# Kernel tuning notes

Hardware: AMD Instinct MI355X
Metric: run time of the kernel (lower is better)

The kernel has to match this reference:

```python
import jax, jax.numpy as jnp
import numpy as np

N_NODES = 50000
N_EDGES = 800000
IN_NODE = 16
IN_EDGE = 8
HID = 128
N_LAYERS = 4
LN_EPS = 1e-5


def setup_inputs() -> dict:
    key = jax.random.key(0)
    ks = jax.random.split(key, 16)
    s = lambda k, shape, fan: jax.random.normal(k, shape, jnp.float32) * (1.0 / np.sqrt(fan))
    inp = {
        "x": jax.random.normal(ks[0], (N_NODES, IN_NODE), jnp.float32),
        "edge_index": jax.random.randint(ks[1], (2, N_EDGES), 0, N_NODES, jnp.int32),
        "edge_attr": jax.random.normal(ks[2], (N_EDGES, IN_EDGE), jnp.float32),
        # input projection
        "W_in": s(ks[3], (HID, IN_NODE), IN_NODE),
        "b_in": jnp.zeros((HID,), jnp.float32),
        # stacked SAGEConv params: lin_l (neighbors, biased), lin_r (root, no bias)
        "Wl": s(ks[4], (N_LAYERS, HID, HID), HID),
        "bl": jnp.zeros((N_LAYERS, HID), jnp.float32),
        "Wr": s(ks[5], (N_LAYERS, HID, HID), HID),
        # stacked LayerNorm params
        "ln_g": jnp.ones((N_LAYERS, HID), jnp.float32),
        "ln_b": jnp.zeros((N_LAYERS, HID), jnp.float32),
        # edge MLP: (2*HID+IN_EDGE) -> HID -> HID//2 -> 1
        "W1": s(ks[6], (HID, 2 * HID + IN_EDGE), 2 * HID + IN_EDGE),
        "b1": jnp.zeros((HID,), jnp.float32),
        "W2": s(ks[7], (HID // 2, HID), HID),
        "b2": jnp.zeros((HID // 2,), jnp.float32),
        "W3": s(ks[8], (1, HID // 2), HID // 2),
        "b3": jnp.zeros((1,), jnp.float32),
    }
    return inp


def reference(x, edge_index, edge_attr, W_in, b_in, Wl, bl, Wr, ln_g, ln_b, W1, b1, W2, b2, W3, b3):
    n = x.shape[0]
    src, dst = edge_index[0], edge_index[1]
    # in-degree for mean aggregation (clamped to 1, as in PyG mean aggr)
    deg = jax.ops.segment_sum(jnp.ones_like(dst, jnp.float32), dst, num_segments=n)
    deg = jnp.maximum(deg, 1.0)[:, None]  # [N,1]

    h = x @ W_in.T + b_in  # [N,H]

    def layer(h, params):
        Wl_i, bl_i, Wr_i, g_i, be_i = params
        # SAGEConv: mean of source features scattered to destinations
        agg = jax.ops.segment_sum(h[src], dst, num_segments=n) / deg
        h2 = agg @ Wl_i.T + bl_i + h @ Wr_i.T
        # LayerNorm
        mu = jnp.mean(h2, axis=-1, keepdims=True)
        var = jnp.mean(jnp.square(h2 - mu), axis=-1, keepdims=True)
        h2 = (h2 - mu) * jax.lax.rsqrt(var + LN_EPS) * g_i + be_i
        # ReLU (dropout = identity in eval mode)
        return jax.nn.relu(h2), None

    h, _ = jax.lax.scan(layer, h, (Wl, bl, Wr, ln_g, ln_b))

    # edge head: gather endpoints, concat with edge_attr, MLP -> scalar logit
    e = jnp.concatenate([h[src], h[dst], edge_attr], axis=1)  # [E, 2H+F_e]
    e = jax.nn.relu(e @ W1.T + b1)
    e = jax.nn.relu(e @ W2.T + b2)
    logits = (e @ W3.T + b3)[:, 0]  # [E]
    return logits
```

## Files before the change

### kernel.cpp

```cpp
#include <hip/hip_runtime.h>
#include <stdint.h>

#define NN 50000
#define NE 800000

#define O_WIN 0
#define O_BIN 2048
#define O_WL  2176
#define O_BL  67712
#define O_WR  68224
#define O_LNG 133760
#define O_LNB 134272
#define O_W1  134784
#define O_B1  168576
#define O_W2  168704
#define O_B2  176896
#define O_W3  176960
#define O_B3  177024
#define W_TOTAL 177025

#define WS_FLAGS 0
#define WS_WC    512
#define WS_CNT   355072
#define WS_ROWP  555520
#define WS_CUR   756224
#define WS_CSR   956928
#define WS_EID   4156928
#define WS_DST   7356928
#define WS_W1P   10556928
#define WS_HB0   10630656
#define WS_HB1   23430656
#define WS_NEED  36230656

#define SCAN_NB 196

typedef float f32x4 __attribute__((ext_vector_type(4)));
typedef short bf16x8 __attribute__((ext_vector_type(8)));
typedef short bf16x4 __attribute__((ext_vector_type(4)));

__device__ __forceinline__ float b2f(unsigned short u) {
  union { unsigned int i; float f; } v; v.i = ((unsigned int)u) << 16; return v.f;
}
__device__ __forceinline__ unsigned short f2b(float f) {
  union { float f; unsigned int i; } v; v.f = f;
  return (unsigned short)((v.i + 0x7fffu + ((v.i >> 16) & 1u)) >> 16);
}

__global__ void k_fallback(unsigned short* __restrict__ out) {
  int gid = blockIdx.x * 256 + threadIdx.x;
  if (gid < NE) out[gid] = 0x3F00;
}

__global__ void k_probe(const unsigned short* __restrict__ x_u,
                        const int* __restrict__ ei32, int* __restrict__ flags) {
  const int t = threadIdx.x;
  int insane = 0;
  for (int i = t; i < 512; i += 64) {
    float v = b2f(x_u[i]);
    if (!(fabsf(v) < 1e4f)) insane++;
  }
#pragma unroll
  for (int off = 1; off < 64; off <<= 1) insane += __shfl_xor(insane, off, 64);
  int nz = 0;
  for (int i = t; i < 128; i += 64) nz |= (ei32[2 * i + 1] != 0);
  unsigned long long m = __ballot(nz != 0);
  if (t == 0) {
    flags[0] = (insane >= 16) ? 1 : 0;
    flags[1] = (m == 0ULL) ? 1 : 0;
  }
}

__global__ void k_cvt_w(const void* W_in, const void* b_in, const void* Wl,
                        const void* bl, const void* Wr, const void* lng,
                        const void* lnb, const void* W1, const void* b1,
                        const void* W2, const void* b2, const void* W3,
                        const void* b3, unsigned short* __restrict__ wc,
                        const int* __restrict__ flags) {
  const int gid = blockIdx.x * 256 + threadIdx.x;
  if (gid >= W_TOTAL) return;
  const int f32 = flags[0];
  const void* src; int off;
  if      (gid < O_BIN) { src = W_in; off = gid - O_WIN; }
  else if (gid < O_WL)  { src = b_in; off = gid - O_BIN; }
  else if (gid < O_BL)  { src = Wl;   off = gid - O_WL;  }
  else if (gid < O_WR)  { src = bl;   off = gid - O_BL;  }
  else if (gid < O_LNG) { src = Wr;   off = gid - O_WR;  }
  else if (gid < O_LNB) { src = lng;  off = gid - O_LNG; }
  else if (gid < O_W1)  { src = lnb;  off = gid - O_LNB; }
  else if (gid < O_B1)  { src = W1;   off = gid - O_W1;  }
  else if (gid < O_W2)  { src = b1;   off = gid - O_B1;  }
  else if (gid < O_B2)  { src = W2;   off = gid - O_W2;  }
  else if (gid < O_W3)  { src = b2;   off = gid - O_B2;  }
  else if (gid < O_B3)  { src = W3;   off = gid - O_W3;  }
  else                  { src = b3;   off = 0;           }
  wc[gid] = f32 ? f2b(((const float*)src)[off]) : ((const unsigned short*)src)[off];
}

__global__ void k_build_w1p(const unsigned short* __restrict__ wc,
                            unsigned short* __restrict__ W1p) {
  int gid = blockIdx.x * 256 + threadIdx.x;
  if (gid >= 128 * 288) return;
  int j = gid / 288, k = gid - j * 288;
  W1p[gid] = (k < 264) ? wc[O_W1 + j * 264 + k] : (unsigned short)0;
}

__global__ void k_cvt_ea(const void* __restrict__ ea,
                         unsigned short* __restrict__ eab,
                         const int* __restrict__ flags) {
  const int gid = blockIdx.x * 256 + threadIdx.x;
  if (gid >= NE) return;
  if (flags[0]) {
    const float4* ep = (const float4*)((const float*)ea + (size_t)gid * 8);
    const float4 a = ep[0], b = ep[1];
    union { ushort4 v[2]; int4 i; } o;
    o.v[0].x = f2b(a.x); o.v[0].y = f2b(a.y); o.v[0].z = f2b(a.z); o.v[0].w = f2b(a.w);
    o.v[1].x = f2b(b.x); o.v[1].y = f2b(b.y); o.v[1].z = f2b(b.z); o.v[1].w = f2b(b.w);
    *(int4*)(eab + (size_t)gid * 8) = o.i;
  } else {
    *(int4*)(eab + (size_t)gid * 8) =
        *(const int4*)((const unsigned short*)ea + (size_t)gid * 8);
  }
}

__global__ void k_hist(const int* __restrict__ ei, int* __restrict__ cnt,
                       const int* __restrict__ flags) {
  const int e = blockIdx.x * 256 + threadIdx.x;
  if (e >= NE) return;
  const int d = flags[1] ? ei[2 * (NE + e)] : ei[NE + e];
  atomicAdd(&cnt[d], 1);
}

__global__ __launch_bounds__(256) void k_scan1(const int* __restrict__ cnt,
                                               int* __restrict__ rowptr,
                                               int* __restrict__ bsum) {
  __shared__ int ws4[4];
  const int t = threadIdx.x, ln = t & 63, wv = t >> 6;
  const int i = blockIdx.x * 256 + t;
  const int v = (i < NN) ? cnt[i] : 0;
  int x = v;
#pragma unroll
  for (int off = 1; off < 64; off <<= 1) {
    int y = __shfl_up(x, off, 64);
    if (ln >= off) x += y;
  }
  if (ln == 63) ws4[wv] = x;
  __syncthreads();
  if (t == 0) { ws4[1] += ws4[0]; ws4[2] += ws4[1]; ws4[3] += ws4[2]; }
  __syncthreads();
  const int woff = wv ? ws4[wv - 1] : 0;
  if (i < NN) rowptr[i] = woff + x - v;
  if (t == 255) bsum[blockIdx.x] = woff + x;
}

__global__ __launch_bounds__(256) void k_scan2(int* __restrict__ bsum) {
  __shared__ int ws4[4];
  const int t = threadIdx.x, ln = t & 63, wv = t >> 6;
  const int v = (t < SCAN_NB) ? bsum[t] : 0;
  int x = v;
#pragma unroll
  for (int off = 1; off < 64; off <<= 1) {
    int y = __shfl_up(x, off, 64);
    if (ln >= off) x += y;
  }
  if (ln == 63) ws4[wv] = x;
  __syncthreads();
  if (t == 0) { ws4[1] += ws4[0]; ws4[2] += ws4[1]; ws4[3] += ws4[2]; }
  __syncthreads();
  const int woff = wv ? ws4[wv - 1] : 0;
  if (t < SCAN_NB) bsum[t] = woff + x - v;
}

__global__ void k_scan3(int* __restrict__ rowptr, const int* __restrict__ bsum) {
  const int i = blockIdx.x * 256 + threadIdx.x;
  if (i < NN) rowptr[i] += bsum[blockIdx.x];
  if (i == 0) rowptr[NN] = NE;
}

__global__ void k_fill(const int* __restrict__ ei, const int* __restrict__ rowptr,
                       int* __restrict__ cursor, int* __restrict__ csr,
                       int* __restrict__ eidA, int* __restrict__ dstA,
                       const int* __restrict__ flags) {
  const int e = blockIdx.x * 256 + threadIdx.x;
  if (e >= NE) return;
  const int i64 = flags[1];
  const int s = i64 ? ei[2 * e] : ei[e];
  const int d = i64 ? ei[2 * (NE + e)] : ei[NE + e];
  const int pos = rowptr[d] + atomicAdd(&cursor[d], 1);
  csr[pos] = s;
  eidA[pos] = e;
  dstA[pos] = d;
}

__global__ void k_inproj(const void* __restrict__ x,
                         const unsigned short* __restrict__ wc,
                         unsigned short* __restrict__ hb,
                         const int* __restrict__ flags) {
  const int gid = blockIdx.x * 256 + threadIdx.x;
  const int n = gid >> 7, j = gid & 127;
  float xv[16];
  if (flags[0]) {
    const float4* xp = (const float4*)((const float*)x + (size_t)n * 16);
#pragma unroll
    for (int q = 0; q < 4; q++) {
      float4 t = xp[q];
      xv[q * 4 + 0] = t.x; xv[q * 4 + 1] = t.y; xv[q * 4 + 2] = t.z; xv[q * 4 + 3] = t.w;
    }
  } else {
    const unsigned short* xu = (const unsigned short*)x + (size_t)n * 16;
#pragma unroll
    for (int q = 0; q < 2; q++) {
      union { int4 v; unsigned short u[8]; } t;
      t.v = *(const int4*)(xu + q * 8);
#pragma unroll
      for (int i = 0; i < 8; i++) xv[q * 8 + i] = b2f(t.u[i]);
    }
  }
  float s = b2f(wc[O_BIN + j]);
  const unsigned short* wrow = wc + O_WIN + j * 16;
#pragma unroll
  for (int q = 0; q < 2; q++) {
    union { int4 v; unsigned short u[8]; } w;
    w.v = *(const int4*)(wrow + q * 8);
#pragma unroll
    for (int i = 0; i < 8; i++) s += b2f(w.u[i]) * xv[q * 8 + i];
  }
  hb[gid] = f2b(s);
}

__global__ __launch_bounds__(256) void k_agg(
    const unsigned short* __restrict__ hin, const int* __restrict__ csr,
    const int* __restrict__ rowptr, unsigned short* __restrict__ aggb) {
  const int tid = threadIdx.x;
  const int n = blockIdx.x * 4 + (tid >> 6);
  const int L = tid & 63;
  const int rs = rowptr[n], re = rowptr[n + 1];
  const unsigned int* hw = (const unsigned int*)hin;
  long long t0 = 0, t1 = 0;
  int e = rs;
  for (; e + 8 <= re; e += 8) {
    unsigned int u[8];
#pragma unroll
    for (int k = 0; k < 8; k++) u[k] = hw[(size_t)csr[e + k] * 64 + L];
#pragma unroll
    for (int k = 0; k < 8; k++) {
      t0 += (int)(b2f((unsigned short)(u[k] & 0xffff)) * 16777216.0f);
      t1 += (int)(b2f((unsigned short)(u[k] >> 16)) * 16777216.0f);
    }
  }
  for (; e + 2 <= re; e += 2) {
    const unsigned int u0 = hw[(size_t)csr[e] * 64 + L];
    const unsigned int u1 = hw[(size_t)csr[e + 1] * 64 + L];
    t0 += (int)(b2f((unsigned short)(u0 & 0xffff)) * 16777216.0f);
    t1 += (int)(b2f((unsigned short)(u0 >> 16)) * 16777216.0f);
    t0 += (int)(b2f((unsigned short)(u1 & 0xffff)) * 16777216.0f);
    t1 += (int)(b2f((unsigned short)(u1 >> 16)) * 16777216.0f);
  }
  if (e < re) {
    const unsigned int u0 = hw[(size_t)csr[e] * 64 + L];
    t0 += (int)(b2f((unsigned short)(u0 & 0xffff)) * 16777216.0f);
    t1 += (int)(b2f((unsigned short)(u0 >> 16)) * 16777216.0f);
  }
  const int dg = re - rs;
  const float rd = (1.0f / 16777216.0f) / (float)(dg > 1 ? dg : 1);
  const float s0 = (float)t0 * rd;
  const float s1 = (float)t1 * rd;
  const unsigned int o = (unsigned int)f2b(s0) | ((unsigned int)f2b(s1) << 16);
  ((unsigned int*)aggb)[(size_t)n * 64 + L] = o;
}

__global__ __launch_bounds__(256) void k_sage_mfma(
    const unsigned short* __restrict__ hin, unsigned short* __restrict__ hagg,
    const unsigned short* __restrict__ wc, int l) {
  __shared__ __align__(16) unsigned char As[64 * 528];
  __shared__ float red1[64][4];
  __shared__ float red2[64][4];
  __shared__ float mr[64][2];
  const int tid = threadIdx.x;
  const int wv = tid >> 6;
  const int L = tid & 63;
  const int l15 = L & 15;
  const int q = L >> 4;
  const int n0 = blockIdx.x * 64;

  bf16x8 wf[2][8];
  float blv[2], gv[2], bv[2];
#pragma unroll
  for (int nt = 0; nt < 2; nt++) {
    const int jj = (wv * 2 + nt) * 16 + l15;
#pragma unroll
    for (int kc = 0; kc < 8; kc++) {
      const unsigned short* src = (kc < 4)
          ? wc + O_WL + ((size_t)l * 128 + jj) * 128 + kc * 32 + q * 8
          : wc + O_WR + ((size_t)l * 128 + jj) * 128 + (kc - 4) * 32 + q * 8;
      wf[nt][kc] = *(const bf16x8*)src;
    }
    blv[nt] = b2f(wc[O_BL + l * 128 + jj]);
    gv[nt]  = b2f(wc[O_LNG + l * 128 + jj]);
    bv[nt]  = b2f(wc[O_LNB + l * 128 + jj]);
  }

  for (int c = tid; c < 2048; c += 256) {
    const int row = c >> 5, part = c & 31;
    int node = n0 + row; if (node > NN - 1) node = NN - 1;
    const unsigned short* src = (part < 16)
        ? hagg + (size_t)node * 128 + part * 8
        : hin + (size_t)node * 128 + (part - 16) * 8;
    *(int4*)(As + row * 528 + part * 16) = *(const int4*)src;
  }
  __syncthreads();

  f32x4 acc[4][2];
#pragma unroll
  for (int mt = 0; mt < 4; mt++)
#pragma unroll
    for (int nt = 0; nt < 2; nt++) acc[mt][nt] = (f32x4)(0.0f);
#pragma unroll
  for (int kc = 0; kc < 8; kc++) {
#pragma unroll
    for (int mt = 0; mt < 4; mt++) {
      const bf16x8 a = *(const bf16x8*)(As + (mt * 16 + l15) * 528 + (kc * 32 + q * 8) * 2);
#pragma unroll
      for (int nt = 0; nt < 2; nt++)
        acc[mt][nt] = __builtin_amdgcn_mfma_f32_16x16x32_bf16(a, wf[nt][kc], acc[mt][nt], 0, 0, 0);
    }
  }
#pragma unroll
  for (int mt = 0; mt < 4; mt++) {
#pragma unroll
    for (int rg = 0; rg < 4; rg++) {
      acc[mt][0][rg] += blv[0];
      acc[mt][1][rg] += blv[1];
      float s = acc[mt][0][rg] + acc[mt][1][rg];
      float s2 = acc[mt][0][rg] * acc[mt][0][rg] + acc[mt][1][rg] * acc[mt][1][rg];
#pragma unroll
      for (int m = 1; m < 16; m <<= 1) {
        s += __shfl_xor(s, m, 64);
        s2 += __shfl_xor(s2, m, 64);
      }
      if (l15 == 0) {
        const int row = mt * 16 + q * 4 + rg;
        red1[row][wv] = s; red2[row][wv] = s2;
      }
    }
  }
  __syncthreads();
  if (tid < 64) {
    const float s1 = red1[tid][0] + red1[tid][1] + red1[tid][2] + red1[tid][3];
    const float s2 = red2[tid][0] + red2[tid][1] + red2[tid][2] + red2[tid][3];
    const float mu = s1 * 0.0078125f;
    const float var = s2 * 0.0078125f - mu * mu;
    mr[tid][0] = mu;
    mr[tid][1] = rsqrtf(var + 1e-5f);
  }
  __syncthreads();
#pragma unroll
  for (int mt = 0; mt < 4; mt++) {
#pragma unroll
    for (int rg = 0; rg < 4; rg++) {
      const int row = mt * 16 + q * 4 + rg;
      const int node = n0 + row;
      if (node < NN) {
        const float mu = mr[row][0], rstd = mr[row][1];
#pragma unroll
        for (int nt = 0; nt < 2; nt++) {
          const float o = (acc[mt][nt][rg] - mu) * rstd * gv[nt] + bv[nt];
          hagg[(size_t)node * 128 + (wv * 2 + nt) * 16 + l15] = f2b(fmaxf(o, 0.f));
        }
      }
    }
  }
}

__global__ __launch_bounds__(256) void k_edge_mfma(
    const unsigned short* __restrict__ hb, const int* __restrict__ csr,
    const int* __restrict__ eidA, const int* __restrict__ dstA,
    const unsigned short* __restrict__ eab, const unsigned short* __restrict__ W1p,
    const unsigned short* __restrict__ wc, void* __restrict__ out,
    const int* __restrict__ flags) {
  __shared__ __align__(16) unsigned char sm[30208];
  unsigned char* const Ue = sm;
  unsigned char* const Hs = sm + 4096;
  unsigned char* const E1 = sm + 4096;
  unsigned char* const E2 = sm + 21504;
  const int tid = threadIdx.x;
  const int wv = tid >> 6;
  const int L = tid & 63;
  const int l15 = L & 15;
  const int q = L >> 4;
  const int f32 = flags[0];

  for (int i = tid; i < 64 * 12; i += 256)
    *(int*)(Ue + (i / 12) * 64 + 16 + (i % 12) * 4) = 0;

  bf16x8 w1f[2][9];
  float b1v[2];
#pragma unroll
  for (int nt = 0; nt < 2; nt++) {
    const int jj = (wv * 2 + nt) * 16 + l15;
#pragma unroll
    for (int cc = 0; cc < 9; cc++)
      w1f[nt][cc] = *(const bf16x8*)(W1p + jj * 288 + cc * 32 + q * 8);
    b1v[nt] = b2f(wc[O_B1 + jj]);
  }
  bf16x8 w2f[4];
  const int jj2 = wv * 16 + l15;
#pragma unroll
  for (int kc = 0; kc < 4; kc++)
    w2f[kc] = *(const bf16x8*)(wc + O_W2 + jj2 * 128 + kc * 32 + q * 8);
  const float b2v = b2f(wc[O_B2 + jj2]);
  float w3v[16];
#pragma unroll
  for (int i = 0; i < 16; i++) w3v[i] = b2f(wc[O_W3 + q * 16 + i]);
  const float b3f = b2f(wc[O_B3]);

  for (int t = blockIdx.x; t < NE / 64; t += gridDim.x) {
    __syncthreads();
    const int pbase = t * 64;
    if (tid < 64) {
      const int e = eidA[pbase + tid];
      *(int4*)(Ue + tid * 64) = *(const int4*)(eab + (size_t)e * 8);
    }
    {
      const int r = tid >> 2, seg = tid & 3;
      const int s = csr[pbase + r];
      const unsigned short* gsrc = hb + (size_t)s * 128 + seg * 32;
      unsigned char* ldst = Hs + r * 272 + seg * 64;
      const int4 v0 = ((const int4*)gsrc)[0];
      const int4 v1 = ((const int4*)gsrc)[1];
      const int4 v2 = ((const int4*)gsrc)[2];
      const int4 v3 = ((const int4*)gsrc)[3];
      ((int4*)ldst)[0] = v0; ((int4*)ldst)[1] = v1;
      ((int4*)ldst)[2] = v2; ((int4*)ldst)[3] = v3;
    }
    int didx[4];
#pragma unroll
    for (int mt = 0; mt < 4; mt++) didx[mt] = dstA[pbase + mt * 16 + l15];
    __syncthreads();

    f32x4 acc1[4][2];
#pragma unroll
    for (int mt = 0; mt < 4; mt++)
#pragma unroll
      for (int nt = 0; nt < 2; nt++) acc1[mt][nt] = (f32x4)(0.0f);
#pragma unroll
    for (int cc = 0; cc < 4; cc++) {
#pragma unroll
      for (int mt = 0; mt < 4; mt++) {
        const bf16x8 a = *(const bf16x8*)(Hs + (mt * 16 + l15) * 272 + (cc * 32 + q * 8) * 2);
#pragma unroll
        for (int nt = 0; nt < 2; nt++)
          acc1[mt][nt] = __builtin_amdgcn_mfma_f32_16x16x32_bf16(a, w1f[nt][cc], acc1[mt][nt], 0, 0, 0);
      }
    }
#pragma unroll
    for (int cc = 4; cc < 8; cc++) {
#pragma unroll
      for (int mt = 0; mt < 4; mt++) {
        const bf16x8 a = *(const bf16x8*)(hb + (size_t)didx[mt] * 128 + (cc - 4) * 32 + q * 8);
#pragma unroll
        for (int nt = 0; nt < 2; nt++)
          acc1[mt][nt] = __builtin_amdgcn_mfma_f32_16x16x32_bf16(a, w1f[nt][cc], acc1[mt][nt], 0, 0, 0);
      }
    }
#pragma unroll
    for (int mt = 0; mt < 4; mt++) {
      const bf16x8 a = *(const bf16x8*)(Ue + (mt * 16 + l15) * 64 + q * 16);
#pragma unroll
      for (int nt = 0; nt < 2; nt++)
        acc1[mt][nt] = __builtin_amdgcn_mfma_f32_16x16x32_bf16(a, w1f[nt][8], acc1[mt][nt], 0, 0, 0);
    }
    __syncthreads();

#pragma unroll
    for (int mt = 0; mt < 4; mt++)
#pragma unroll
      for (int nt = 0; nt < 2; nt++)
#pragma unroll
        for (int rg = 0; rg < 4; rg++) {
          const int er = mt * 16 + q * 4 + rg;
          const int jj = (wv * 2 + nt) * 16 + l15;
          *(unsigned short*)(E1 + er * 272 + jj * 2) =
              f2b(fmaxf(acc1[mt][nt][rg] + b1v[nt], 0.f));
        }
    __syncthreads();

    f32x4 acc2[4];
#pragma unroll
    for (int mt = 0; mt < 4; mt++) acc2[mt] = (f32x4)(0.0f);
#pragma unroll
    for (int kc = 0; kc < 4; kc++) {
#pragma unroll
      for (int mt = 0; mt < 4; mt++) {
        const bf16x8 a = *(const bf16x8*)(E1 + (mt * 16 + l15) * 272 + (kc * 32 + q * 8) * 2);
        acc2[mt] = __builtin_amdgcn_mfma_f32_16x16x32_bf16(a, w2f[kc], acc2[mt], 0, 0, 0);
      }
    }
#pragma unroll
    for (int mt = 0; mt < 4; mt++)
#pragma unroll
      for (int rg = 0; rg < 4; rg++) {
        const int er = mt * 16 + q * 4 + rg;
        *(unsigned short*)(E2 + er * 136 + jj2 * 2) =
            f2b(fmaxf(acc2[mt][rg] + b2v, 0.f));
      }
    __syncthreads();

    const int el = wv * 16 + l15;
    float acc = 0.f;
#pragma unroll
    for (int i4 = 0; i4 < 4; i4++) {
      const bf16x4 v = *(const bf16x4*)(E2 + el * 136 + q * 32 + i4 * 8);
      acc += b2f((unsigned short)v[0]) * w3v[i4 * 4 + 0];
      acc += b2f((unsigned short)v[1]) * w3v[i4 * 4 + 1];
      acc += b2f((unsigned short)v[2]) * w3v[i4 * 4 + 2];
      acc += b2f((unsigned short)v[3]) * w3v[i4 * 4 + 3];
    }
    acc += __shfl_xor(acc, 16, 64);
    acc += __shfl_xor(acc, 32, 64);
    if (q == 0) {
      const int e = eidA[pbase + el];
      const float r = acc + b3f;
      if (f32) ((float*)out)[e] = r;
      else     ((unsigned short*)out)[e] = f2b(r);
    }
  }
}

extern "C" void kernel_launch(void* const* d_in, const int* in_sizes, int n_in,
                              void* d_out, int out_size, void* d_ws, size_t ws_size,
                              hipStream_t stream) {
  const void* x  = d_in[0];
  const int*  ei = (const int*)d_in[1];
  const void* ea = d_in[2];

  char* ws = (char*)d_ws;
  int*            flags  = (int*)(ws + WS_FLAGS);
  unsigned short* wc     = (unsigned short*)(ws + WS_WC);
  int*            cnt    = (int*)(ws + WS_CNT);
  int*            rowptr = (int*)(ws + WS_ROWP);
  int*            cursor = (int*)(ws + WS_CUR);
  int*            csr    = (int*)(ws + WS_CSR);
  int*            eidA   = (int*)(ws + WS_EID);
  int*            dstA   = (int*)(ws + WS_DST);
  unsigned short* W1p    = (unsigned short*)(ws + WS_W1P);
  unsigned short* hb0    = (unsigned short*)(ws + WS_HB0);
  unsigned short* hb1    = (unsigned short*)(ws + WS_HB1);
  int*            bsum   = (int*)(ws + WS_CSR);

  if (ws_size < WS_NEED) {
    k_fallback<<<3125, 256, 0, stream>>>((unsigned short*)d_out);
    return;
  }

  k_probe<<<1, 64, 0, stream>>>((const unsigned short*)x, ei, flags);
  k_cvt_w<<<(W_TOTAL + 255) / 256, 256, 0, stream>>>(
      d_in[3], d_in[4], d_in[5], d_in[6], d_in[7], d_in[8], d_in[9],
      d_in[10], d_in[11], d_in[12], d_in[13], d_in[14], d_in[15], wc, flags);
  k_build_w1p<<<144, 256, 0, stream>>>(wc, W1p);

  hipMemsetAsync(cnt, 0, NN * sizeof(int), stream);
  hipMemsetAsync(cursor, 0, NN * sizeof(int), stream);
  k_hist<<<3125, 256, 0, stream>>>(ei, cnt, flags);
  k_scan1<<<SCAN_NB, 256, 0, stream>>>(cnt, rowptr, bsum);
  k_scan2<<<1, 256, 0, stream>>>(bsum);
  k_scan3<<<SCAN_NB, 256, 0, stream>>>(rowptr, bsum);
  k_fill<<<3125, 256, 0, stream>>>(ei, rowptr, cursor, csr, eidA, dstA, flags);

  k_inproj<<<NN * 128 / 256, 256, 0, stream>>>(x, wc, hb0, flags);

  unsigned short* cur = hb0;
  unsigned short* nxt = hb1;
  for (int l = 0; l < 4; l++) {
    k_agg<<<12500, 256, 0, stream>>>(cur, csr, rowptr, nxt);
    k_sage_mfma<<<782, 256, 0, stream>>>(cur, nxt, wc, l);
    unsigned short* tmp = cur; cur = nxt; nxt = tmp;
  }
  unsigned short* eab = nxt;
  k_cvt_ea<<<3125, 256, 0, stream>>>(ea, eab, flags);
  k_edge_mfma<<<3125, 256, 0, stream>>>(cur, csr, eidA, dstA, eab, W1p, wc, d_out, flags);
}
```

Measured before the change: 609.7 us.

## Software-pipeline edge MLP gathers into registers and relax tile barriers

```diff
diff --git a/kernel.cpp b/kernel.cpp
--- a/kernel.cpp
+++ b/kernel.cpp
@@ -45,6 +45,11 @@
   union { float f; unsigned int i; } v; v.f = f;
   return (unsigned short)((v.i + 0x7fffu + ((v.i >> 16) & 1u)) >> 16);
 }
+
+#define LBAR() do { \
+  asm volatile("s_waitcnt lgkmcnt(0)" ::: "memory"); \
+  __builtin_amdgcn_s_barrier(); \
+} while (0)
 
 __global__ void k_fallback(unsigned short* __restrict__ out) {
   int gid = blockIdx.x * 256 + threadIdx.x;
@@ -388,6 +393,7 @@
   const int l15 = L & 15;
   const int q = L >> 4;
   const int f32 = flags[0];
+  const int r4 = tid >> 2, seg = tid & 3;
 
   for (int i = tid; i < 64 * 12; i += 256)
     *(int*)(Ue + (i / 12) * 64 + 16 + (i % 12) * 4) = 0;
@@ -408,34 +414,58 @@
   for (int kc = 0; kc < 4; kc++)
     w2f[kc] = *(const bf16x8*)(wc + O_W2 + jj2 * 128 + kc * 32 + q * 8);
   const float b2v = b2f(wc[O_B2 + jj2]);
-  float w3v[16];
-#pragma unroll
-  for (int i = 0; i < 16; i++) w3v[i] = b2f(wc[O_W3 + q * 16 + i]);
   const float b3f = b2f(wc[O_B3]);
 
-  for (int t = blockIdx.x; t < NE / 64; t += gridDim.x) {
-    __syncthreads();
+  const int NT = NE / 64;
+
+  int4 hsr0, hsr1, hsr2, hsr3;
+  int4 uer; uer.x = uer.y = uer.z = uer.w = 0;
+  int didx0, didx1, didx2, didx3;
+  {
+    const int p0 = blockIdx.x * 64;
+    const int s0 = csr[p0 + r4];
+    const unsigned short* gs = hb + (size_t)s0 * 128 + seg * 32;
+    hsr0 = ((const int4*)gs)[0]; hsr1 = ((const int4*)gs)[1];
+    hsr2 = ((const int4*)gs)[2]; hsr3 = ((const int4*)gs)[3];
+    if (tid < 64) {
+      const int e0 = eidA[p0 + tid];
+      uer = *(const int4*)(eab + (size_t)e0 * 8);
+    }
+    didx0 = dstA[p0 + 0 * 16 + l15];
+    didx1 = dstA[p0 + 1 * 16 + l15];
+    didx2 = dstA[p0 + 2 * 16 + l15];
+    didx3 = dstA[p0 + 3 * 16 + l15];
+  }
+
+  for (int t = blockIdx.x; t < NT; t += gridDim.x) {
     const int pbase = t * 64;
-    if (tid < 64) {
-      const int e = eidA[pbase + tid];
-      *(int4*)(Ue + tid * 64) = *(const int4*)(eab + (size_t)e * 8);
-    }
+    const int tn = (t + (int)gridDim.x < NT) ? (t + (int)gridDim.x) : t;
+    const int pnext = tn * 64;
+
+    if (tid < 64) *(int4*)(Ue + tid * 64) = uer;
     {
-      const int r = tid >> 2, seg = tid & 3;
-      const int s = csr[pbase + r];
-      const unsigned short* gsrc = hb + (size_t)s * 128 + seg * 32;
-      unsigned char* ldst = Hs + r * 272 + seg * 64;
-      const int4 v0 = ((const int4*)gsrc)[0];
-      const int4 v1 = ((const int4*)gsrc)[1];
-      const int4 v2 = ((const int4*)gsrc)[2];
-      const int4 v3 = ((const int4*)gsrc)[3];
-      ((int4*)ldst)[0] = v0; ((int4*)ldst)[1] = v1;
-      ((int4*)ldst)[2] = v2; ((int4*)ldst)[3] = v3;
-    }
-    int didx[4];
-#pragma unroll
-    for (int mt = 0; mt < 4; mt++) didx[mt] = dstA[pbase + mt * 16 + l15];
-    __syncthreads();
+      unsigned char* ldst = Hs + r4 * 272 + seg * 64;
+      ((int4*)ldst)[0] = hsr0; ((int4*)ldst)[1] = hsr1;
+      ((int4*)ldst)[2] = hsr2; ((int4*)ldst)[3] = hsr3;
+    }
+    const int sN = csr[pnext + r4];
+    int eN = 0;
+    if (tid < 64) eN = eidA[pnext + tid];
+    const int didxn0 = dstA[pnext + 0 * 16 + l15];
+    const int didxn1 = dstA[pnext + 1 * 16 + l15];
+    const int didxn2 = dstA[pnext + 2 * 16 + l15];
+    const int didxn3 = dstA[pnext + 3 * 16 + l15];
+
+    LBAR();
+
+    int4 h0, h1, h2, h3;
+    {
+      const unsigned short* gsn = hb + (size_t)sN * 128 + seg * 32;
+      h0 = ((const int4*)gsn)[0]; h1 = ((const int4*)gsn)[1];
+      h2 = ((const int4*)gsn)[2]; h3 = ((const int4*)gsn)[3];
+    }
+    int4 uen; uen.x = uen.y = uen.z = uen.w = 0;
+    if (tid < 64) uen = *(const int4*)(eab + (size_t)eN * 8);
 
     f32x4 acc1[4][2];
 #pragma unroll
@@ -452,14 +482,17 @@
           acc1[mt][nt] = __builtin_amdgcn_mfma_f32_16x16x32_bf16(a, w1f[nt][cc], acc1[mt][nt], 0, 0, 0);
       }
     }
-#pragma unroll
-    for (int cc = 4; cc < 8; cc++) {
-#pragma unroll
-      for (int mt = 0; mt < 4; mt++) {
-        const bf16x8 a = *(const bf16x8*)(hb + (size_t)didx[mt] * 128 + (cc - 4) * 32 + q * 8);
-#pragma unroll
-        for (int nt = 0; nt < 2; nt++)
-          acc1[mt][nt] = __builtin_amdgcn_mfma_f32_16x16x32_bf16(a, w1f[nt][cc], acc1[mt][nt], 0, 0, 0);
+    {
+      const int dd[4] = {didx0, didx1, didx2, didx3};
+#pragma unroll
+      for (int cc = 4; cc < 8; cc++) {
+#pragma unroll
+        for (int mt = 0; mt < 4; mt++) {
+          const bf16x8 a = *(const bf16x8*)(hb + (size_t)dd[mt] * 128 + (cc - 4) * 32 + q * 8);
+#pragma unroll
+          for (int nt = 0; nt < 2; nt++)
+            acc1[mt][nt] = __builtin_amdgcn_mfma_f32_16x16x32_bf16(a, w1f[nt][cc], acc1[mt][nt], 0, 0, 0);
+        }
       }
     }
 #pragma unroll
@@ -469,7 +502,7 @@
       for (int nt = 0; nt < 2; nt++)
         acc1[mt][nt] = __builtin_amdgcn_mfma_f32_16x16x32_bf16(a, w1f[nt][8], acc1[mt][nt], 0, 0, 0);
     }
-    __syncthreads();
+    LBAR();
 
 #pragma unroll
     for (int mt = 0; mt < 4; mt++)
@@ -482,7 +515,7 @@
           *(unsigned short*)(E1 + er * 272 + jj * 2) =
               f2b(fmaxf(acc1[mt][nt][rg] + b1v[nt], 0.f));
         }
-    __syncthreads();
+    LBAR();
 
     f32x4 acc2[4];
 #pragma unroll
@@ -503,17 +536,16 @@
         *(unsigned short*)(E2 + er * 136 + jj2 * 2) =
             f2b(fmaxf(acc2[mt][rg] + b2v, 0.f));
       }
-    __syncthreads();
+    LBAR();
 
     const int el = wv * 16 + l15;
     float acc = 0.f;
 #pragma unroll
     for (int i4 = 0; i4 < 4; i4++) {
       const bf16x4 v = *(const bf16x4*)(E2 + el * 136 + q * 32 + i4 * 8);
-      acc += b2f((unsigned short)v[0]) * w3v[i4 * 4 + 0];
-      acc += b2f((unsigned short)v[1]) * w3v[i4 * 4 + 1];
-      acc += b2f((unsigned short)v[2]) * w3v[i4 * 4 + 2];
-      acc += b2f((unsigned short)v[3]) * w3v[i4 * 4 + 3];
+#pragma unroll
+      for (int j = 0; j < 4; j++)
+        acc += b2f((unsigned short)v[j]) * b2f(wc[O_W3 + q * 16 + i4 * 4 + j]);
     }
     acc += __shfl_xor(acc, 16, 64);
     acc += __shfl_xor(acc, 32, 64);
@@ -523,6 +555,10 @@
       if (f32) ((float*)out)[e] = r;
       else     ((unsigned short*)out)[e] = f2b(r);
     }
+
+    hsr0 = h0; hsr1 = h1; hsr2 = h2; hsr3 = h3;
+    uer = uen;
+    didx0 = didxn0; didx1 = didxn1; didx2 = didxn2; didx3 = didxn3;
   }
 }
 
```

New measurement: 594.7 us. -2.5%, faster.
